# Performance work log

Hardware: AMD Instinct MI355X
Metric: run time of the kernel (lower is better)

The kernel has to match this reference:

```python
import jax, jax.numpy as jnp
import numpy as np

HEIGHT = 108
WIDTH = 108
LEN_CLASSES = 7
EPS = 1e-5


def layout_bbox(pred, H, W):
    # pred: [B, O, 4 + LEN_CLASSES]
    bbox = pred[..., :4]
    cls_prob = pred[..., 4:]  # [B,O,7]
    x_c = bbox[..., 0] * W   # [B,O]
    y_c = bbox[..., 1] * H
    w = bbox[..., 2] * W
    h = bbox[..., 3] * H
    x1 = (x_c - 0.5 * w)[:, :, None, None]  # [B,O,1,1]
    x2 = (x_c + 0.5 * w)[:, :, None, None]
    y1 = (y_c - 0.5 * h)[:, :, None, None]
    y2 = (y_c + 0.5 * h)[:, :, None, None]
    xt = jnp.arange(W, dtype=pred.dtype)[None, None, None, :]  # [1,1,1,W]
    yt = jnp.arange(H, dtype=pred.dtype)[None, None, :, None]  # [1,1,H,1]
    x1d = xt - x1  # [B,O,1,W]
    x2d = x2 - xt
    y1d = yt - y1  # [B,O,H,1]
    y2d = y2 - yt
    # min(relu(d), 1) == clip(d, 0, 1)
    yband = jnp.clip(y1d, 0.0, 1.0) * jnp.clip(y2d, 0.0, 1.0)  # [B,O,H,1]
    xband = jnp.clip(x1d, 0.0, 1.0) * jnp.clip(x2d, 0.0, 1.0)  # [B,O,1,W]
    x1_line = jax.nn.relu(1.0 - jnp.abs(x1d)) * yband  # [B,O,H,W]
    x2_line = jax.nn.relu(1.0 - jnp.abs(x2d)) * yband
    y1_line = jax.nn.relu(1.0 - jnp.abs(y1d)) * xband
    y2_line = jax.nn.relu(1.0 - jnp.abs(y2d)) * xband
    xy_max = jnp.maximum(jnp.maximum(x1_line, x2_line), jnp.maximum(y1_line, y2_line))  # [B,O,H,W]
    spatial = xy_max[..., None] * cls_prob[:, :, None, None, :]  # [B,O,H,W,7]
    return jnp.max(spatial, axis=1)  # [B,H,W,7]


def bn(x, g, b, axes):
    m = jnp.mean(x, axis=axes, keepdims=True)
    v = jnp.var(x, axis=axes, keepdims=True)
    shape = [1] * x.ndim
    shape[1 if x.ndim == 4 else -1] = -1
    return (x - m) * jax.lax.rsqrt(v + EPS) * g.reshape(shape) + b.reshape(shape)


def conv2d(x, w, b, stride):
    y = jax.lax.conv_general_dilated(x, w, (stride, stride), 'VALID',
                                     dimension_numbers=('NCHW', 'OIHW', 'NCHW'))
    return y + b[None, :, None, None]


def setup_inputs() -> dict:
    key = jax.random.key(0)
    ks = jax.random.split(key, 16)
    B, O = 64, 16
    d = {}
    d['image'] = jax.random.uniform(ks[0], (B, O, 4 + LEN_CLASSES), dtype=jnp.float32)
    d['conv1_w'] = jax.random.normal(ks[1], (32, LEN_CLASSES, 5, 5), jnp.float32) * 0.05
    d['conv1_b'] = jnp.zeros((32,), jnp.float32)
    d['bn1_g'] = jnp.ones((32,), jnp.float32)
    d['bn1_b'] = jnp.zeros((32,), jnp.float32)
    d['conv2_w'] = jax.random.normal(ks[2], (64, 32, 5, 5), jnp.float32) * 0.03
    d['conv2_b'] = jnp.zeros((64,), jnp.float32)
    d['bn2_g'] = jnp.ones((64,), jnp.float32)
    d['bn2_b'] = jnp.zeros((64,), jnp.float32)
    d['fc1_w'] = jax.random.normal(ks[3], (512, 36864), jnp.float32) * 0.005
    d['fc1_b'] = jnp.zeros((512,), jnp.float32)
    d['bn3_g'] = jnp.ones((512,), jnp.float32)
    d['bn3_b'] = jnp.zeros((512,), jnp.float32)
    d['fc2_w'] = jax.random.normal(ks[4], (1, 512), jnp.float32) * 0.04
    d['fc2_b'] = jnp.zeros((1,), jnp.float32)
    return d


def reference(image, conv1_w, conv1_b, bn1_g, bn1_b, conv2_w, conv2_b, bn2_g, bn2_b,
              fc1_w, fc1_b, bn3_g, bn3_b, fc2_w, fc2_b):
    # layout_bbox(image, WIDTH, HEIGHT): output_height=WIDTH, output_width=HEIGHT (both 108)
    layout = layout_bbox(image, WIDTH, HEIGHT)           # [B,108,108,7]
    x = jnp.transpose(layout, (0, 3, 1, 2))              # [B,7,108,108]
    x = conv2d(x, conv1_w, conv1_b, 2)                   # [B,32,52,52]
    x = bn(x, bn1_g, bn1_b, (0, 2, 3))
    x = jax.nn.leaky_relu(x, 0.2)
    x = conv2d(x, conv2_w, conv2_b, 2)                   # [B,64,24,24]
    x = bn(x, bn2_g, bn2_b, (0, 2, 3))
    x = jax.nn.leaky_relu(x, 0.2)
    x = x.reshape(x.shape[0], -1)                        # [B,36864]
    x = x @ fc1_w.T + fc1_b                              # [B,512]
    x = bn(x, bn3_g, bn3_b, (0,))
    x = jax.nn.leaky_relu(x, 0.2)
    x = x @ fc2_w.T + fc2_b                              # [B,1]
    return jax.nn.sigmoid(x)
```

## Files before the change

kernel.cpp:

```cpp
#include <hip/hip_runtime.h>
#include <hip/hip_bf16.h>


typedef unsigned short u16;
typedef __attribute__((ext_vector_type(8))) short bf8_t;
typedef __attribute__((ext_vector_type(4))) float f4_t;
#define MFMA16(a, b, c) __builtin_amdgcn_mfma_f32_16x16x32_bf16(a, b, c, 0, 0, 0)

#define LEAKY(v) (fmaxf((v), 0.2f * (v)))
#define CLIP01(v) fminf(fmaxf((v), 0.0f), 1.0f)

__device__ inline unsigned f2bf(float f) {
  unsigned u = __float_as_uint(f);
  return (u + 0x7FFFu + ((u >> 16) & 1u)) >> 16;
}
__device__ inline float bf2f(unsigned u) { return __uint_as_float(u << 16); }

constexpr int HW = 108;
constexpr int NOBJ = 16;
constexpr int NCLS = 7;

__global__ __launch_bounds__(128) void layout_kernel(
    const float* __restrict__ image, u16* __restrict__ lay8) {
  int h = blockIdx.x, b = blockIdx.y;
  __shared__ float sIm[NOBJ * 11];
  int tid = threadIdx.x;
  for (int i = tid; i < NOBJ * 11; i += 128) sIm[i] = image[b * NOBJ * 11 + i];
  __syncthreads();
  int w = tid;
  if (w >= HW) return;
  float best[NCLS];
#pragma unroll
  for (int c = 0; c < NCLS; ++c) best[c] = 0.0f;
  float fw = (float)w, fh = (float)h;
  for (int o = 0; o < NOBJ; ++o) {
    const float* p = &sIm[o * 11];
    float xc = p[0] * 108.0f, yc = p[1] * 108.0f;
    float wd = p[2] * 108.0f, hd = p[3] * 108.0f;
    float x1 = xc - 0.5f * wd, x2 = xc + 0.5f * wd;
    float y1 = yc - 0.5f * hd, y2 = yc + 0.5f * hd;
    float x1d = fw - x1, x2d = x2 - fw;
    float y1d = fh - y1, y2d = y2 - fh;
    float yband = CLIP01(y1d) * CLIP01(y2d);
    float xband = CLIP01(x1d) * CLIP01(x2d);
    float x1l = fmaxf(1.0f - fabsf(x1d), 0.0f) * yband;
    float x2l = fmaxf(1.0f - fabsf(x2d), 0.0f) * yband;
    float y1l = fmaxf(1.0f - fabsf(y1d), 0.0f) * xband;
    float y2l = fmaxf(1.0f - fabsf(y2d), 0.0f) * xband;
    float xy = fmaxf(fmaxf(x1l, x2l), fmaxf(y1l, y2l));
#pragma unroll
    for (int c = 0; c < NCLS; ++c) best[c] = fmaxf(best[c], xy * p[4 + c]);
  }
  unsigned p0 = f2bf(best[0]) | (f2bf(best[1]) << 16);
  unsigned p1 = f2bf(best[2]) | (f2bf(best[3]) << 16);
  unsigned p2 = f2bf(best[4]) | (f2bf(best[5]) << 16);
  unsigned p3 = f2bf(best[6]);
  uint4 st = {p0, p1, p2, p3};
  ((uint4*)lay8)[b * 11664 + h * 108 + w] = st;
}

__global__ __launch_bounds__(256) void wprep_kernel(
    const float* __restrict__ w1, const float* __restrict__ w2,
    u16* __restrict__ wB1, u16* __restrict__ wB2, float* __restrict__ st) {
  int i = blockIdx.x * 256 + threadIdx.x;
  if (i < 1216) st[i] = 0.f;
  if (i < 7168) {
    int co = i / 224, k = i % 224;
    int chunk = k >> 5, kk = k & 31, tl = kk >> 3, ci = kk & 7;
    int tap = chunk * 4 + tl;
    unsigned v = 0;
    if (tap < 25 && ci < 7) v = f2bf(w1[co * 175 + ci * 25 + tap]);
    wB1[i] = (u16)v;
  } else if (i < 58368) {
    int j = i - 7168;
    int tap = j / 2048, r = j % 2048, co = r >> 5, ci = r & 31;
    wB2[j] = (u16)f2bf(w2[co * 800 + ci * 25 + tap]);
  }
}

__global__ __launch_bounds__(128) void conv1_mfma(
    const u16* __restrict__ lay8, const u16* __restrict__ wB1,
    u16* __restrict__ x1r, float* __restrict__ bn1sum,
    float* __restrict__ bn1sq) {
  int mtg = blockIdx.x, nt = blockIdx.y, bz = blockIdx.z;
  int tid = threadIdx.x;
  int lane = tid & 63, wv = tid >> 6;
  int f = lane & 15, q = lane >> 4;
  int co = nt * 16 + f;
  int b0 = bz * 4 + wv * 2;
  int pbase[4];
  bool mvalid[4];
#pragma unroll
  for (int t = 0; t < 4; ++t) {
    int mt = mtg * 4 + t;
    mvalid[t] = mt < 169;
    int P = min(mt * 16 + f, 2703);
    int oh = P / 52, ow = P - oh * 52;
    pbase[t] = (oh * 2 * 108 + ow * 2) * 8;
  }
  f4_t acc[2][4];
#pragma unroll
  for (int b2 = 0; b2 < 2; ++b2)
#pragma unroll
    for (int t = 0; t < 4; ++t) acc[b2][t] = {0.f, 0.f, 0.f, 0.f};
#pragma unroll
  for (int chunk = 0; chunk < 7; ++chunk) {
    int tap = chunk * 4 + q;
    tap = tap > 24 ? 24 : tap;
    int kh = tap / 5, kw = tap - kh * 5;
    int toff = (kh * 108 + kw) * 8;
    bf8_t bf = *(const bf8_t*)&wB1[co * 224 + chunk * 32 + q * 8];
#pragma unroll
    for (int b2 = 0; b2 < 2; ++b2) {
      const u16* lb = lay8 + (size_t)(b0 + b2) * 93312;
#pragma unroll
      for (int t = 0; t < 4; ++t) {
        bf8_t af = *(const bf8_t*)&lb[pbase[t] + toff];
        acc[b2][t] = MFMA16(af, bf, acc[b2][t]);
      }
    }
  }
  float s = 0.f, sq = 0.f;
#pragma unroll
  for (int b2 = 0; b2 < 2; ++b2) {
    u16* ob = x1r + (size_t)(b0 + b2) * 86528;
#pragma unroll
    for (int t = 0; t < 4; ++t) {
      if (!mvalid[t]) continue;
      int P0 = (mtg * 4 + t) * 16 + q * 4;
#pragma unroll
      for (int r = 0; r < 4; ++r) {
        float v = acc[b2][t][r];
        s += v;
        sq += v * v;
        ob[(P0 + r) * 32 + co] = (u16)f2bf(v);
      }
    }
  }
  s += __shfl_xor(s, 16);
  s += __shfl_xor(s, 32);
  sq += __shfl_xor(sq, 16);
  sq += __shfl_xor(sq, 32);
  __shared__ float rs[2][16], rq[2][16];
  if (lane < 16) {
    rs[wv][f] = s;
    rq[wv][f] = sq;
  }
  __syncthreads();
  if (tid < 16) {
    atomicAdd(&bn1sum[nt * 16 + tid], rs[0][tid] + rs[1][tid]);
    atomicAdd(&bn1sq[nt * 16 + tid], rq[0][tid] + rq[1][tid]);
  }
}

__global__ __launch_bounds__(256) void bnapply1_kernel(
    const u16* __restrict__ x1r, const float* __restrict__ bn1sum,
    const float* __restrict__ bn1sq, const float* __restrict__ g1,
    const float* __restrict__ b1, u16* __restrict__ x1b) {
  int idx = blockIdx.x * 256 + threadIdx.x;
  int base = idx * 8, c0 = base & 31;
  float sc[8], sh[8];
#pragma unroll
  for (int j = 0; j < 8; ++j) {
    int c = c0 + j;
    float mean = bn1sum[c] * (1.f / 173056.f);
    float var = bn1sq[c] * (1.f / 173056.f) - mean * mean;
    float s = g1[c] * rsqrtf(var + 1e-5f);
    sc[j] = s;
    sh[j] = b1[c] - mean * s;
  }
  uint4 in = *(const uint4*)&x1r[base];
  unsigned w[4] = {in.x, in.y, in.z, in.w};
  unsigned out[4];
#pragma unroll
  for (int j = 0; j < 4; ++j) {
    float a = bf2f(w[j] & 0xffffu);
    float bq = bf2f(w[j] >> 16);
    a = LEAKY(fmaf(a, sc[2 * j], sh[2 * j]));
    bq = LEAKY(fmaf(bq, sc[2 * j + 1], sh[2 * j + 1]));
    out[j] = f2bf(a) | (f2bf(bq) << 16);
  }
  uint4 st = {out[0], out[1], out[2], out[3]};
  *(uint4*)&x1b[base] = st;
}

__global__ __launch_bounds__(256) void conv2_mfma(
    const u16* __restrict__ x1b, const u16* __restrict__ wB2,
    float* __restrict__ x2c, float* __restrict__ bn2sum,
    float* __restrict__ bn2sq) {
  int mt = blockIdx.x, nt = blockIdx.y, bz = blockIdx.z;
  int tid = threadIdx.x;
  int lane = tid & 63, wv = tid >> 6;
  int f = lane & 15, q = lane >> 4;
  int co = nt * 16 + f;
  int b0 = bz * 16 + wv * 4;
  int P = mt * 16 + f;
  int oh = P / 24, ow = P - oh * 24;
  int abase = (oh * 2 * 52 + ow * 2) * 32 + q * 8;
  f4_t acc[4];
#pragma unroll
  for (int b2 = 0; b2 < 4; ++b2) acc[b2] = {0.f, 0.f, 0.f, 0.f};
#pragma unroll
  for (int tap = 0; tap < 25; ++tap) {
    int kh = tap / 5, kw = tap - kh * 5;
    int toff = (kh * 52 + kw) * 32;
    bf8_t bf = *(const bf8_t*)&wB2[tap * 2048 + co * 32 + q * 8];
#pragma unroll
    for (int b2 = 0; b2 < 4; ++b2) {
      bf8_t af =
          *(const bf8_t*)&x1b[(size_t)(b0 + b2) * 86528 + abase + toff];
      acc[b2] = MFMA16(af, bf, acc[b2]);
    }
  }
  float s = 0.f, sq = 0.f;
#pragma unroll
  for (int b2 = 0; b2 < 4; ++b2) {
    float* ob = x2c + (size_t)(b0 + b2) * 36864;
#pragma unroll
    for (int r = 0; r < 4; ++r) {
      float v = acc[b2][r];
      s += v;
      sq += v * v;
      ob[(mt * 16 + q * 4 + r) * 64 + co] = v;
    }
  }
  s += __shfl_xor(s, 16);
  s += __shfl_xor(s, 32);
  sq += __shfl_xor(sq, 16);
  sq += __shfl_xor(sq, 32);
  __shared__ float rs[4][16], rq[4][16];
  if (lane < 16) {
    rs[wv][f] = s;
    rq[wv][f] = sq;
  }
  __syncthreads();
  if (tid < 16) {
    atomicAdd(&bn2sum[nt * 16 + tid],
              rs[0][tid] + rs[1][tid] + rs[2][tid] + rs[3][tid]);
    atomicAdd(&bn2sq[nt * 16 + tid],
              rq[0][tid] + rq[1][tid] + rq[2][tid] + rq[3][tid]);
  }
}

__global__ __launch_bounds__(256) void bnapply2t_kernel(
    const float* __restrict__ x2c, const float* __restrict__ bn2sum,
    const float* __restrict__ bn2sq, const float* __restrict__ g2,
    const float* __restrict__ b2, u16* __restrict__ xB) {
  int hw0 = blockIdx.x * 64, b = blockIdx.y;
  __shared__ float tile[64 * 65];
  int t = threadIdx.x;
  int c = t & 63, hl4 = t >> 6;
  float mean = bn2sum[c] * (1.f / 36864.f);
  float var = bn2sq[c] * (1.f / 36864.f) - mean * mean;
  float s = g2[c] * rsqrtf(var + 1e-5f);
  float h = b2[c] - mean * s;
#pragma unroll
  for (int it = 0; it < 16; ++it) {
    int hl = it * 4 + hl4;
    float v = x2c[((size_t)b * 576 + hw0 + hl) * 64 + c];
    tile[hl * 65 + c] = LEAKY(fmaf(v, s, h));
  }
  __syncthreads();
  int hw = t & 63, cl4 = t >> 6;
#pragma unroll
  for (int it = 0; it < 16; ++it) {
    int cc = it * 4 + cl4;
    xB[(size_t)b * 36864 + cc * 576 + hw0 + hw] = (u16)f2bf(tile[hw * 65 + cc]);
  }
}

__global__ __launch_bounds__(256) void fc1_mfma(
    const u16* __restrict__ xB, const float* __restrict__ wgt,
    float* __restrict__ part) {
  int ks = blockIdx.x, nb = blockIdx.y;
  int tid = threadIdx.x;
  int lane = tid & 63, wv = tid >> 6;
  int f = lane & 15, q = lane >> 4;
  int n0 = nb * 64 + wv * 16;
  int kbase = ks * 512;
  __shared__ u16 sA[64 * 520];
#pragma unroll
  for (int i = 0; i < 16; ++i) {
    int c = i * 256 + tid;
    int row = c >> 6, col = c & 63;
    *(uint4*)&sA[row * 520 + col * 8] =
        *(const uint4*)&xB[(size_t)row * 36864 + kbase + col * 8];
  }
  __syncthreads();
  f4_t acc[4];
#pragma unroll
  for (int m = 0; m < 4; ++m) acc[m] = {0.f, 0.f, 0.f, 0.f};
  const float* wrow = wgt + (size_t)(n0 + f) * 36864 + kbase + q * 8;
#pragma unroll 4
  for (int kt = 0; kt < 16; ++kt) {
    const float* wp = wrow + kt * 32;
    float4 wa = *(const float4*)wp;
    float4 wb = *(const float4*)(wp + 4);
    union { bf8_t v; u16 u[8]; } bu;
    bu.u[0] = (u16)f2bf(wa.x); bu.u[1] = (u16)f2bf(wa.y);
    bu.u[2] = (u16)f2bf(wa.z); bu.u[3] = (u16)f2bf(wa.w);
    bu.u[4] = (u16)f2bf(wb.x); bu.u[5] = (u16)f2bf(wb.y);
    bu.u[6] = (u16)f2bf(wb.z); bu.u[7] = (u16)f2bf(wb.w);
    bf8_t afr[4];
#pragma unroll
    for (int m = 0; m < 4; ++m)
      afr[m] = *(const bf8_t*)&sA[(m * 16 + f) * 520 + kt * 32 + q * 8];
#pragma unroll
    for (int m = 0; m < 4; ++m) acc[m] = MFMA16(afr[m], bu.v, acc[m]);
  }
  float* pp = part + (size_t)ks * 32768;
#pragma unroll
  for (int m = 0; m < 4; ++m)
#pragma unroll
    for (int r = 0; r < 4; ++r)
      pp[(m * 16 + q * 4 + r) * 512 + n0 + f] = acc[m][r];
}

__global__ __launch_bounds__(256) void fc1_reduce_kernel(
    const float* __restrict__ part, float* __restrict__ fc1o,
    float* __restrict__ bn3sum, float* __restrict__ bn3sq) {
  int i = blockIdx.x * 256 + threadIdx.x;
  float s = 0.f;
#pragma unroll 8
  for (int ks = 0; ks < 72; ++ks) s += part[(size_t)ks * 32768 + i];
  fc1o[i] = s;
  atomicAdd(&bn3sum[i & 511], s);
  atomicAdd(&bn3sq[i & 511], s * s);
}

__global__ __launch_bounds__(64) void fc2_kernel(
    const float* __restrict__ fc1o, const float* __restrict__ bn3sum,
    const float* __restrict__ bn3sq, const float* __restrict__ g3,
    const float* __restrict__ b3, const float* __restrict__ w2,
    const float* __restrict__ b2o, float* __restrict__ out) {
  int m = blockIdx.x;
  int fl = threadIdx.x;
  float a = 0.f;
#pragma unroll
  for (int j = 0; j < 8; ++j) {
    int ff = fl + j * 64;
    float mean = bn3sum[ff] * (1.f / 64.f);
    float var = bn3sq[ff] * (1.f / 64.f) - mean * mean;
    float sc = g3[ff] * rsqrtf(var + 1e-5f);
    float sh = b3[ff] - mean * sc;
    float v = LEAKY(fmaf(fc1o[m * 512 + ff], sc, sh));
    a += v * w2[ff];
  }
  for (int off = 32; off; off >>= 1) a += __shfl_down(a, off, 64);
  if (fl == 0) out[m] = 1.f / (1.f + expf(-(a + b2o[0])));
}

extern "C" void kernel_launch(void* const* d_in, const int* in_sizes, int n_in,
                              void* d_out, int out_size, void* d_ws,
                              size_t ws_size, hipStream_t stream) {
  const float* image = (const float*)d_in[0];
  const float* c1w = (const float*)d_in[1];
  const float* bn1g = (const float*)d_in[3];
  const float* bn1b = (const float*)d_in[4];
  const float* c2w = (const float*)d_in[5];
  const float* bn2g = (const float*)d_in[7];
  const float* bn2b = (const float*)d_in[8];
  const float* f1w = (const float*)d_in[9];
  const float* bn3g = (const float*)d_in[11];
  const float* bn3b = (const float*)d_in[12];
  const float* f2w = (const float*)d_in[13];
  const float* f2b = (const float*)d_in[14];
  float* ws = (float*)d_ws;

  u16* lay8 = (u16*)ws;
  u16* x1r = (u16*)(ws + 2985984);
  u16* x1b = (u16*)(ws + 5754880);
  float* x2c = ws + 8523776;
  u16* xB = (u16*)(ws + 10883072);
  float* fc1part = ws + 12062720;
  float* fc1o = ws + 14422016;
  float* st = ws + 14454784;
  float* bn1sum = st, *bn1sq = st + 32;
  float* bn2sum = st + 64, *bn2sq = st + 128;
  float* bn3sum = st + 192, *bn3sq = st + 704;
  u16* wB1 = (u16*)(ws + 14456000);
  u16* wB2 = (u16*)(ws + 14459584);

  wprep_kernel<<<228, 256, 0, stream>>>(c1w, c2w, wB1, wB2, st);
  layout_kernel<<<dim3(108, 64), 128, 0, stream>>>(image, lay8);
  conv1_mfma<<<dim3(43, 2, 16), 128, 0, stream>>>(lay8, wB1, x1r, bn1sum,
                                                  bn1sq);
  bnapply1_kernel<<<2704, 256, 0, stream>>>(x1r, bn1sum, bn1sq, bn1g, bn1b,
                                            x1b);
  conv2_mfma<<<dim3(36, 4, 4), 256, 0, stream>>>(x1b, wB2, x2c, bn2sum,
                                                 bn2sq);
  bnapply2t_kernel<<<dim3(9, 64), 256, 0, stream>>>(x2c, bn2sum, bn2sq, bn2g,
                                                    bn2b, xB);
  fc1_mfma<<<dim3(72, 8), 256, 0, stream>>>(xB, f1w, fc1part);
  fc1_reduce_kernel<<<128, 256, 0, stream>>>(fc1part, fc1o, bn3sum, bn3sq);
  fc2_kernel<<<64, 64, 0, stream>>>(fc1o, bn3sum, bn3sq, bn3g, bn3b, f2w, f2b,
                                    (float*)d_out);
}
```

Before: 254.9 us.

## Fuse weight prep into layout kernel, double conv2 and fc1 grid parallelism

Folds the weight-conversion and stats-zeroing work into the first 114 blocks of the layout kernel, removing one launch. Conv2 now handles 2 batches per wave instead of 4, doubling the grid along z. fc1 splits K into 256-element slices (144 slices) and reads activations directly from global memory instead of staging them in LDS. The aim is more blocks in flight for these memory-bound stages; the costs are a larger partial-sum buffer and a longer reduction for fc1, plus uncoalesced global activation reads.

```diff
diff --git a/kernel.cpp b/kernel.cpp
--- a/kernel.cpp
+++ b/kernel.cpp
@@ -20,11 +20,33 @@
 constexpr int NOBJ = 16;
 constexpr int NCLS = 7;
 
-__global__ __launch_bounds__(128) void layout_kernel(
-    const float* __restrict__ image, u16* __restrict__ lay8) {
+__global__ __launch_bounds__(128) void layout_prep_kernel(
+    const float* __restrict__ image, const float* __restrict__ w1,
+    const float* __restrict__ w2, u16* __restrict__ lay8,
+    u16* __restrict__ wB1, u16* __restrict__ wB2, float* __restrict__ st) {
   int h = blockIdx.x, b = blockIdx.y;
+  int tid = threadIdx.x;
+  int bid = b * 108 + h;
+  if (bid < 114) {
+#pragma unroll
+    for (int j = 0; j < 4; ++j) {
+      int i = bid * 512 + j * 128 + tid;
+      if (i < 1216) st[i] = 0.f;
+      if (i < 7168) {
+        int co = i / 224, k = i % 224;
+        int chunk = k >> 5, kk = k & 31, tl = kk >> 3, ci = kk & 7;
+        int tap = chunk * 4 + tl;
+        unsigned v = 0;
+        if (tap < 25 && ci < 7) v = f2bf(w1[co * 175 + ci * 25 + tap]);
+        wB1[i] = (u16)v;
+      } else if (i < 58368) {
+        int jj = i - 7168;
+        int tap = jj / 2048, r = jj % 2048, co = r >> 5, ci = r & 31;
+        wB2[jj] = (u16)f2bf(w2[co * 800 + ci * 25 + tap]);
+      }
+    }
+  }
   __shared__ float sIm[NOBJ * 11];
-  int tid = threadIdx.x;
   for (int i = tid; i < NOBJ * 11; i += 128) sIm[i] = image[b * NOBJ * 11 + i];
   __syncthreads();
   int w = tid;
@@ -55,27 +77,8 @@
   unsigned p1 = f2bf(best[2]) | (f2bf(best[3]) << 16);
   unsigned p2 = f2bf(best[4]) | (f2bf(best[5]) << 16);
   unsigned p3 = f2bf(best[6]);
-  uint4 st = {p0, p1, p2, p3};
-  ((uint4*)lay8)[b * 11664 + h * 108 + w] = st;
-}
-
-__global__ __launch_bounds__(256) void wprep_kernel(
-    const float* __restrict__ w1, const float* __restrict__ w2,
-    u16* __restrict__ wB1, u16* __restrict__ wB2, float* __restrict__ st) {
-  int i = blockIdx.x * 256 + threadIdx.x;
-  if (i < 1216) st[i] = 0.f;
-  if (i < 7168) {
-    int co = i / 224, k = i % 224;
-    int chunk = k >> 5, kk = k & 31, tl = kk >> 3, ci = kk & 7;
-    int tap = chunk * 4 + tl;
-    unsigned v = 0;
-    if (tap < 25 && ci < 7) v = f2bf(w1[co * 175 + ci * 25 + tap]);
-    wB1[i] = (u16)v;
-  } else if (i < 58368) {
-    int j = i - 7168;
-    int tap = j / 2048, r = j % 2048, co = r >> 5, ci = r & 31;
-    wB2[j] = (u16)f2bf(w2[co * 800 + ci * 25 + tap]);
-  }
+  uint4 stv = {p0, p1, p2, p3};
+  ((uint4*)lay8)[b * 11664 + h * 108 + w] = stv;
 }
 
 __global__ __launch_bounds__(128) void conv1_mfma(
@@ -180,8 +183,8 @@
     bq = LEAKY(fmaf(bq, sc[2 * j + 1], sh[2 * j + 1]));
     out[j] = f2bf(a) | (f2bf(bq) << 16);
   }
-  uint4 st = {out[0], out[1], out[2], out[3]};
-  *(uint4*)&x1b[base] = st;
+  uint4 stv = {out[0], out[1], out[2], out[3]};
+  *(uint4*)&x1b[base] = stv;
 }
 
 __global__ __launch_bounds__(256) void conv2_mfma(
@@ -193,20 +196,20 @@
   int lane = tid & 63, wv = tid >> 6;
   int f = lane & 15, q = lane >> 4;
   int co = nt * 16 + f;
-  int b0 = bz * 16 + wv * 4;
+  int b0 = bz * 8 + wv * 2;
   int P = mt * 16 + f;
   int oh = P / 24, ow = P - oh * 24;
   int abase = (oh * 2 * 52 + ow * 2) * 32 + q * 8;
-  f4_t acc[4];
-#pragma unroll
-  for (int b2 = 0; b2 < 4; ++b2) acc[b2] = {0.f, 0.f, 0.f, 0.f};
+  f4_t acc[2];
+#pragma unroll
+  for (int b2 = 0; b2 < 2; ++b2) acc[b2] = {0.f, 0.f, 0.f, 0.f};
 #pragma unroll
   for (int tap = 0; tap < 25; ++tap) {
     int kh = tap / 5, kw = tap - kh * 5;
     int toff = (kh * 52 + kw) * 32;
     bf8_t bf = *(const bf8_t*)&wB2[tap * 2048 + co * 32 + q * 8];
 #pragma unroll
-    for (int b2 = 0; b2 < 4; ++b2) {
+    for (int b2 = 0; b2 < 2; ++b2) {
       bf8_t af =
           *(const bf8_t*)&x1b[(size_t)(b0 + b2) * 86528 + abase + toff];
       acc[b2] = MFMA16(af, bf, acc[b2]);
@@ -214,7 +217,7 @@
   }
   float s = 0.f, sq = 0.f;
 #pragma unroll
-  for (int b2 = 0; b2 < 4; ++b2) {
+  for (int b2 = 0; b2 < 2; ++b2) {
     float* ob = x2c + (size_t)(b0 + b2) * 36864;
 #pragma unroll
     for (int r = 0; r < 4; ++r) {
@@ -277,22 +280,14 @@
   int lane = tid & 63, wv = tid >> 6;
   int f = lane & 15, q = lane >> 4;
   int n0 = nb * 64 + wv * 16;
-  int kbase = ks * 512;
-  __shared__ u16 sA[64 * 520];
-#pragma unroll
-  for (int i = 0; i < 16; ++i) {
-    int c = i * 256 + tid;
-    int row = c >> 6, col = c & 63;
-    *(uint4*)&sA[row * 520 + col * 8] =
-        *(const uint4*)&xB[(size_t)row * 36864 + kbase + col * 8];
-  }
-  __syncthreads();
+  int kbase = ks * 256;
   f4_t acc[4];
 #pragma unroll
   for (int m = 0; m < 4; ++m) acc[m] = {0.f, 0.f, 0.f, 0.f};
   const float* wrow = wgt + (size_t)(n0 + f) * 36864 + kbase + q * 8;
-#pragma unroll 4
-  for (int kt = 0; kt < 16; ++kt) {
+  const u16* arow = xB + kbase + q * 8;
+#pragma unroll
+  for (int kt = 0; kt < 8; ++kt) {
     const float* wp = wrow + kt * 32;
     float4 wa = *(const float4*)wp;
     float4 wb = *(const float4*)(wp + 4);
@@ -304,7 +299,7 @@
     bf8_t afr[4];
 #pragma unroll
     for (int m = 0; m < 4; ++m)
-      afr[m] = *(const bf8_t*)&sA[(m * 16 + f) * 520 + kt * 32 + q * 8];
+      afr[m] = *(const bf8_t*)&arow[(size_t)(m * 16 + f) * 36864 + kt * 32];
 #pragma unroll
     for (int m = 0; m < 4; ++m) acc[m] = MFMA16(afr[m], bu.v, acc[m]);
   }
@@ -322,7 +317,7 @@
   int i = blockIdx.x * 256 + threadIdx.x;
   float s = 0.f;
 #pragma unroll 8
-  for (int ks = 0; ks < 72; ++ks) s += part[(size_t)ks * 32768 + i];
+  for (int ks = 0; ks < 144; ++ks) s += part[(size_t)ks * 32768 + i];
   fc1o[i] = s;
   atomicAdd(&bn3sum[i & 511], s);
   atomicAdd(&bn3sq[i & 511], s * s);
@@ -373,25 +368,25 @@
   float* x2c = ws + 8523776;
   u16* xB = (u16*)(ws + 10883072);
   float* fc1part = ws + 12062720;
-  float* fc1o = ws + 14422016;
-  float* st = ws + 14454784;
+  float* fc1o = ws + 16781312;
+  float* st = ws + 16814080;
   float* bn1sum = st, *bn1sq = st + 32;
   float* bn2sum = st + 64, *bn2sq = st + 128;
   float* bn3sum = st + 192, *bn3sq = st + 704;
-  u16* wB1 = (u16*)(ws + 14456000);
-  u16* wB2 = (u16*)(ws + 14459584);
-
-  wprep_kernel<<<228, 256, 0, stream>>>(c1w, c2w, wB1, wB2, st);
-  layout_kernel<<<dim3(108, 64), 128, 0, stream>>>(image, lay8);
+  u16* wB1 = (u16*)(ws + 16815296);
+  u16* wB2 = (u16*)(ws + 16818880);
+
+  layout_prep_kernel<<<dim3(108, 64), 128, 0, stream>>>(image, c1w, c2w, lay8,
+                                                        wB1, wB2, st);
   conv1_mfma<<<dim3(43, 2, 16), 128, 0, stream>>>(lay8, wB1, x1r, bn1sum,
                                                   bn1sq);
   bnapply1_kernel<<<2704, 256, 0, stream>>>(x1r, bn1sum, bn1sq, bn1g, bn1b,
                                             x1b);
-  conv2_mfma<<<dim3(36, 4, 4), 256, 0, stream>>>(x1b, wB2, x2c, bn2sum,
+  conv2_mfma<<<dim3(36, 4, 8), 256, 0, stream>>>(x1b, wB2, x2c, bn2sum,
                                                  bn2sq);
   bnapply2t_kernel<<<dim3(9, 64), 256, 0, stream>>>(x2c, bn2sum, bn2sq, bn2g,
                                                     bn2b, xB);
-  fc1_mfma<<<dim3(72, 8), 256, 0, stream>>>(xB, f1w, fc1part);
+  fc1_mfma<<<dim3(144, 8), 256, 0, stream>>>(xB, f1w, fc1part);
   fc1_reduce_kernel<<<128, 256, 0, stream>>>(fc1part, fc1o, bn3sum, bn3sq);
   fc2_kernel<<<64, 64, 0, stream>>>(fc1o, bn3sum, bn3sq, bn3g, bn3b, f2w, f2b,
                                     (float*)d_out);
```

Measured after the change: 265.6 us. +4.2%, slower.
